# Optimization experiments

Measured on AMD Instinct MI355X. Metric: run time of the kernel, lower is better.

Reference implementation:

```python
import jax, jax.numpy as jnp
import numpy as np

IN_SIZE = 256
OUT_SIZE = 256
WIN = 2  # window_size


def setup_inputs() -> dict:
    key = jax.random.key(0)
    k1, k2 = jax.random.split(key)
    x = jax.random.normal(k1, (8, 4096, IN_SIZE), dtype=jnp.float32)
    W = jax.random.normal(k2, (3 * OUT_SIZE, WIN * IN_SIZE), dtype=jnp.float32) * 0.05
    b = jnp.zeros((3 * OUT_SIZE,), dtype=jnp.float32)
    return {"x": x, "W": W, "b": b}


def reference(x, W, b):
    bsz, seq_len, _ = x.shape
    toks = [x]
    for i in range(WIN - 1):
        shifted = jnp.concatenate(
            [jnp.zeros((bsz, i + 1, IN_SIZE), x.dtype), x[:, : -(i + 1), :]], axis=1
        )
        toks.insert(0, shifted)
    xw = jnp.stack(toks, axis=2).reshape(bsz, seq_len, WIN * IN_SIZE)

    # Gated projection: z (update), f (forget), o (output)
    y = xw @ W.T + b  # (B, S, 3*OUT)
    z, f, o = jnp.split(y, 3, axis=2)
    z = jnp.tanh(z)
    f = jax.nn.sigmoid(f)

    # fo-pooling recurrence: c_t = f_t * c_{t-1} + (1 - f_t) * z_t
    def step(c, fz):
        ft, zt = fz
        c = ft * c + (1.0 - ft) * zt
        return c, c

    fz = (jnp.swapaxes(f, 0, 1), jnp.swapaxes(z, 0, 1))  # (S, B, OUT)
    c0 = jnp.zeros((bsz, OUT_SIZE), z.dtype)
    _, cs = jax.lax.scan(step, c0, fz)
    c = jnp.swapaxes(cs, 0, 1)  # (B, S, OUT)

    return jax.nn.sigmoid(o) * c
```

## Files before the change

### kernel.cpp

```cpp
#include <hip/hip_runtime.h>
#include <cstdint>
#include <cstddef>

#define BATCH  8
#define SEQ    4096
#define CHN    256
#define NQ     768
#define KTOT   512
#define TS     128
#define NCHUNK (SEQ/TS)
#define SROW   4097

typedef __attribute__((ext_vector_type(8))) __bf16    bf16x8;
typedef __attribute__((ext_vector_type(4))) float     f32x4;
typedef __attribute__((ext_vector_type(4))) _Float16  f16x4;
typedef __attribute__((ext_vector_type(2))) _Float16  f16x2;

#define AS1(p) ((const __attribute__((address_space(1))) void*)(p))
#define AS3(p) ((__attribute__((address_space(3))) void*)(p))

__global__ __launch_bounds__(256) void k_convW(const float* __restrict__ W,
                                               __bf16* __restrict__ Wt) {
    int lin = blockIdx.x * 256 + threadIdx.x;
    int n  = lin % NQ;
    int tg = lin / NQ;
    const float* src = W + (size_t)n * KTOT + tg * 8;
    float4 a = *(const float4*)(src);
    float4 b = *(const float4*)(src + 4);
    bf16x8 h;
    h[0]=(__bf16)a.x; h[1]=(__bf16)a.y; h[2]=(__bf16)a.z; h[3]=(__bf16)a.w;
    h[4]=(__bf16)b.x; h[5]=(__bf16)b.y; h[6]=(__bf16)b.z; h[7]=(__bf16)b.w;
    *(bf16x8*)(Wt + (size_t)lin * 8) = h;
}

__global__ __launch_bounds__(256) void k_convX(const float* __restrict__ x,
                                               __bf16* __restrict__ Xb) {
    int c = blockIdx.x * 256 + threadIdx.x;
    if (c < 8 * 32) {
        int bz = c >> 5, j = c & 31;
        bf16x8 zz = {};
        *(bf16x8*)(Xb + (size_t)bz * SROW * 256 + j * 8) = zz;
    }
    int bi = c >> 17;
    int r  = c & 131071;
    int s  = r >> 5;
    int j  = r & 31;
    const float* src = x + ((size_t)bi * SEQ + s) * 256 + j * 8;
    float4 a = *(const float4*)(src);
    float4 b = *(const float4*)(src + 4);
    bf16x8 h;
    h[0]=(__bf16)a.x; h[1]=(__bf16)a.y; h[2]=(__bf16)a.z; h[3]=(__bf16)a.w;
    h[4]=(__bf16)b.x; h[5]=(__bf16)b.y; h[6]=(__bf16)b.z; h[7]=(__bf16)b.w;
    *(bf16x8*)(Xb + ((size_t)bi * SROW + 1 + s) * 256 + j * 8) = h;
}

__device__ __forceinline__ float fast_sigmoid(float y) {
    float e = __expf(-y);
    return __builtin_amdgcn_rcpf(1.f + e);
}
__device__ __forceinline__ float fast_tanh(float y) {
    float e = __expf(-2.f * y);
    return __builtin_amdgcn_rcpf(1.f + e) * 2.f - 1.f;
}

__global__ __launch_bounds__(256, 3) void k_gemm(
    const __bf16* __restrict__ Xb, const __bf16* __restrict__ Wt,
    const float* __restrict__ bias,
    _Float16* __restrict__ Zb, _Float16* __restrict__ Fb, _Float16* __restrict__ Ob)
{
    __shared__ char XL[2][16384];
    __shared__ char WL[2][8192];

    int tid = threadIdx.x;
    int bid = blockIdx.x;
    int x_  = bid & 7;
    int i_  = bid >> 3;
    int ngt = i_ % 6;
    int sbt = (i_ / 6) * 8 + x_;
    int bi  = sbt >> 5;
    int sc  = sbt & 31;
    int s0  = sc * 128;
    int wid = tid >> 6;
    int l   = tid & 63;
    int l15 = l & 15, lg = l >> 4;
    int wr  = wid >> 1;
    int wc  = wid & 1;

    #define STAGE_X(bsel, q)                                                     \
        {                                                                        \
            _Pragma("unroll")                                                    \
            for (int i2 = 0; i2 < 4; ++i2) {                                     \
                int slot = i2 * 256 + tid;                                       \
                int row  = slot >> 3;                                            \
                int c16  = slot & 7;                                             \
                int c16g = c16 ^ (row & 7);                                      \
                const __bf16* gsrc = Xb +                                        \
                    ((size_t)bi * SROW + s0 + row + ((q) >> 2)) * 256            \
                    + ((q) & 3) * 64 + c16g * 8;                                 \
                __builtin_amdgcn_global_load_lds(AS1(gsrc),                      \
                    AS3(XL[bsel] + slot * 16), 16, 0, 0);                        \
            }                                                                    \
        }
    #define STAGE_W(bsel, t)                                                     \
        {                                                                        \
            _Pragma("unroll")                                                    \
            for (int i2 = 0; i2 < 2; ++i2) {                                     \
                int slot = i2 * 256 + tid;                                       \
                int p  = slot >> 7;                                              \
                int nl = slot & 127;                                             \
                const __bf16* gsrc = Wt +                                        \
                    ((size_t)((t) * 4 + p) * NQ + ngt * 128 + nl) * 8;           \
                __builtin_amdgcn_global_load_lds(AS1(gsrc),                      \
                    AS3(WL[bsel] + slot * 16), 16, 0, 0);                        \
            }                                                                    \
        }

    f32x4 acc[4][4];
    const f32x4 vzero = {0.f, 0.f, 0.f, 0.f};
    #pragma unroll
    for (int a = 0; a < 4; ++a)
        #pragma unroll
        for (int b = 0; b < 4; ++b)
            acc[a][b] = vzero;

    STAGE_X(0, 0);
    STAGE_W(0, 0);
    __syncthreads();

    #pragma unroll
    for (int t = 0; t < 16; ++t) {
        if (t < 15) {
            STAGE_W((t + 1) & 1, t + 1);
            if (t & 1) STAGE_X(((t + 1) >> 1) & 1, (t + 1) >> 1);
        }

        const char* Xc = XL[(t >> 1) & 1];
        const char* Wc = WL[t & 1];
        bf16x8 xf[4], wf[4];
        #pragma unroll
        for (int st = 0; st < 4; ++st) {
            int row = wr * 64 + st * 16 + l15;
            int byte = (row * 128 + ((t & 1) * 4 + lg) * 16) ^ ((row & 7) << 4);
            xf[st] = *(const bf16x8*)(Xc + byte);
        }
        #pragma unroll
        for (int nt = 0; nt < 4; ++nt)
            wf[nt] = *(const bf16x8*)(Wc + lg * 2048
                                         + (wc * 64 + nt * 16 + l15) * 16);
        __builtin_amdgcn_s_setprio(1);
        #pragma unroll
        for (int nt = 0; nt < 4; ++nt)
            #pragma unroll
            for (int st = 0; st < 4; ++st)
                acc[nt][st] = __builtin_amdgcn_mfma_f32_16x16x32_bf16(
                                  wf[nt], xf[st], acc[nt][st], 0, 0, 0);
        __builtin_amdgcn_s_setprio(0);

        __syncthreads();
    }

    int gate    = ngt >> 1;
    int ch_base = (ngt & 1) * 128 + wc * 64;
    _Float16* buf = (gate == 0) ? Zb : (gate == 1) ? Fb : Ob;
    char* Sw = (char*)XL + wid * 8192;

    #pragma unroll
    for (int nt = 0; nt < 4; ++nt) {
        float4 bv = *(const float4*)(bias + ngt * 128 + wc * 64 + nt * 16 + lg * 4);
        #pragma unroll
        for (int st = 0; st < 4; ++st) {
            f16x4 hv;
            #pragma unroll
            for (int r = 0; r < 4; ++r) {
                float bvr = (r == 0) ? bv.x : (r == 1) ? bv.y : (r == 2) ? bv.z : bv.w;
                float y = acc[nt][st][r] + bvr;
                float v = (gate == 0) ? fast_tanh(y) : fast_sigmoid(y);
                hv[r] = (_Float16)v;
            }
            int byte = ((st * 16 + l15) * 128 + (nt * 16 + lg * 4) * 2)
                       ^ ((l15 & 7) << 4);
            *(f16x4*)(Sw + byte) = hv;
        }
    }
    #pragma unroll
    for (int so = 0; so < 16; ++so) {
        int s_loc = so * 4 + lg;
        int byte  = (s_loc * 128 + l15 * 8) ^ ((s_loc & 7) << 4);
        f16x4 v = *(const f16x4*)(Sw + byte);
        *(f16x4*)(buf + ((size_t)bi * SEQ + s0 + wr * 64 + s_loc) * CHN
                      + ch_base + l15 * 4) = v;
    }
}

__global__ __launch_bounds__(128) void k_scan1(const _Float16* __restrict__ Fb,
                                               const _Float16* __restrict__ Zb,
                                               float* __restrict__ Aq,
                                               float* __restrict__ Bq) {
    int bi = blockIdx.x >> 5;
    int ck = blockIdx.x & 31;
    int c2 = threadIdx.x;
    size_t base = (((size_t)bi * SEQ + ck * TS) * CHN + c2 * 2) >> 1;
    const f16x2* F2 = (const f16x2*)Fb;
    const f16x2* Z2 = (const f16x2*)Zb;
    float a0 = 1.f, a1 = 1.f, c0 = 0.f, c1 = 0.f;
    #pragma unroll 8
    for (int s = 0; s < TS; ++s) {
        f16x2 f = F2[base + (size_t)s * (CHN / 2)];
        f16x2 z = Z2[base + (size_t)s * (CHN / 2)];
        float f0 = (float)f[0], f1 = (float)f[1];
        c0 = f0 * c0 + (1.f - f0) * (float)z[0];
        c1 = f1 * c1 + (1.f - f1) * (float)z[1];
        a0 *= f0; a1 *= f1;
    }
    int o = blockIdx.x * CHN + c2 * 2;
    *(float2*)(Aq + o) = make_float2(a0, a1);
    *(float2*)(Bq + o) = make_float2(c0, c1);
}

__global__ __launch_bounds__(256) void k_scan2(const float* __restrict__ Aq,
                                               const float* __restrict__ Bq,
                                               float* __restrict__ Cq) {
    int bi = blockIdx.x;
    int ch = threadIdx.x;
    float c = 0.f;
    #pragma unroll
    for (int ck = 0; ck < NCHUNK; ++ck) {
        int o = (bi * NCHUNK + ck) * CHN + ch;
        Cq[o] = c;
        c = Aq[o] * c + Bq[o];
    }
}

__global__ __launch_bounds__(128) void k_scan3(const _Float16* __restrict__ Fb,
                                               const _Float16* __restrict__ Zb,
                                               const _Float16* __restrict__ Ob,
                                               const float* __restrict__ Cq,
                                               float* __restrict__ out) {
    int bi = blockIdx.x >> 5;
    int ck = blockIdx.x & 31;
    int c2 = threadIdx.x;
    float2 c = *(const float2*)(Cq + blockIdx.x * CHN + c2 * 2);
    size_t base = (((size_t)bi * SEQ + ck * TS) * CHN + c2 * 2) >> 1;
    const f16x2* F2 = (const f16x2*)Fb;
    const f16x2* Z2 = (const f16x2*)Zb;
    const f16x2* O2 = (const f16x2*)Ob;
    float* outp = out + (((size_t)bi * SEQ + ck * TS) * CHN + c2 * 2);
    #pragma unroll 4
    for (int s = 0; s < TS; ++s) {
        f16x2 f  = F2[base + (size_t)s * (CHN / 2)];
        f16x2 z  = Z2[base + (size_t)s * (CHN / 2)];
        f16x2 so = O2[base + (size_t)s * (CHN / 2)];
        float f0 = (float)f[0], f1 = (float)f[1];
        c.x = f0 * c.x + (1.f - f0) * (float)z[0];
        c.y = f1 * c.y + (1.f - f1) * (float)z[1];
        *(float2*)(outp + (size_t)s * CHN) = make_float2((float)so[0] * c.x,
                                                         (float)so[1] * c.y);
    }
}

extern "C" void kernel_launch(void* const* d_in, const int* in_sizes, int n_in,
                              void* d_out, int out_size, void* d_ws, size_t ws_size,
                              hipStream_t stream)
{
    const float* x = (const float*)d_in[0];
    const float* W = (const float*)d_in[1];
    const float* b = (const float*)d_in[2];
    float* out = (float*)d_out;

    char* ws = (char*)d_ws;
    const size_t MB = 1024 * 1024;
    _Float16* Zb = (_Float16*)(ws +  0 * MB);
    _Float16* Fb = (_Float16*)(ws + 16 * MB);
    _Float16* Ob = (_Float16*)(ws + 32 * MB);
    __bf16*   Wt = (__bf16*)  (ws + 48 * MB);
    float*    Aq = (float*)   (ws + 49 * MB);
    float*    Bq = (float*)   (ws + 50 * MB);
    float*    Cq = (float*)   (ws + 51 * MB);
    __bf16*   Xb = (__bf16*)  (ws + 52 * MB);

    k_convW<<<dim3(192),            dim3(256), 0, stream>>>(W, Wt);
    k_convX<<<dim3(4096),           dim3(256), 0, stream>>>(x, Xb);
    k_gemm <<<dim3(1536),           dim3(256), 0, stream>>>(Xb, Wt, b, Zb, Fb, Ob);
    k_scan1<<<dim3(BATCH * NCHUNK), dim3(128), 0, stream>>>(Fb, Zb, Aq, Bq);
    k_scan2<<<dim3(BATCH),          dim3(256), 0, stream>>>(Aq, Bq, Cq);
    k_scan3<<<dim3(BATCH * NCHUNK), dim3(128), 0, stream>>>(Fb, Zb, Ob, Cq, out);
}
```

Baseline: 78.72 us.

## Fuse fp32-to-bf16 X conversion into GEMM staging and halve sequence tile

Removes the separate X conversion kernel. The GEMM now loads fp32 x directly into registers, handles the shifted window with a zero row at the sequence start, converts to bf16 and writes the result to LDS after the MFMAs. The sequence tile is halved to 64 rows, which doubles the GEMM grid and the scan chunk count, and launch bounds are raised to 4 blocks per CU. This saves an intermediate bf16 buffer round trip and a launch. In exchange the X path goes through registers instead of direct global-to-LDS loads, global traffic per tile is doubled, and each block has a smaller MFMA tile with more W reloads.

```diff
diff --git a/kernel.cpp b/kernel.cpp
--- a/kernel.cpp
+++ b/kernel.cpp
@@ -7,9 +7,8 @@
 #define CHN    256
 #define NQ     768
 #define KTOT   512
-#define TS     128
+#define TS     64
 #define NCHUNK (SEQ/TS)
-#define SROW   4097
 
 typedef __attribute__((ext_vector_type(8))) __bf16    bf16x8;
 typedef __attribute__((ext_vector_type(4))) float     f32x4;
@@ -33,27 +32,6 @@
     *(bf16x8*)(Wt + (size_t)lin * 8) = h;
 }
 
-__global__ __launch_bounds__(256) void k_convX(const float* __restrict__ x,
-                                               __bf16* __restrict__ Xb) {
-    int c = blockIdx.x * 256 + threadIdx.x;
-    if (c < 8 * 32) {
-        int bz = c >> 5, j = c & 31;
-        bf16x8 zz = {};
-        *(bf16x8*)(Xb + (size_t)bz * SROW * 256 + j * 8) = zz;
-    }
-    int bi = c >> 17;
-    int r  = c & 131071;
-    int s  = r >> 5;
-    int j  = r & 31;
-    const float* src = x + ((size_t)bi * SEQ + s) * 256 + j * 8;
-    float4 a = *(const float4*)(src);
-    float4 b = *(const float4*)(src + 4);
-    bf16x8 h;
-    h[0]=(__bf16)a.x; h[1]=(__bf16)a.y; h[2]=(__bf16)a.z; h[3]=(__bf16)a.w;
-    h[4]=(__bf16)b.x; h[5]=(__bf16)b.y; h[6]=(__bf16)b.z; h[7]=(__bf16)b.w;
-    *(bf16x8*)(Xb + ((size_t)bi * SROW + 1 + s) * 256 + j * 8) = h;
-}
-
 __device__ __forceinline__ float fast_sigmoid(float y) {
     float e = __expf(-y);
     return __builtin_amdgcn_rcpf(1.f + e);
@@ -63,12 +41,12 @@
     return __builtin_amdgcn_rcpf(1.f + e) * 2.f - 1.f;
 }
 
-__global__ __launch_bounds__(256, 3) void k_gemm(
-    const __bf16* __restrict__ Xb, const __bf16* __restrict__ Wt,
+__global__ __launch_bounds__(256, 4) void k_gemm(
+    const float* __restrict__ x, const __bf16* __restrict__ Wt,
     const float* __restrict__ bias,
     _Float16* __restrict__ Zb, _Float16* __restrict__ Fb, _Float16* __restrict__ Ob)
 {
-    __shared__ char XL[2][16384];
+    __shared__ char XL[2][8192];
     __shared__ char WL[2][8192];
 
     int tid = threadIdx.x;
@@ -77,53 +55,65 @@
     int i_  = bid >> 3;
     int ngt = i_ % 6;
     int sbt = (i_ / 6) * 8 + x_;
-    int bi  = sbt >> 5;
-    int sc  = sbt & 31;
-    int s0  = sc * 128;
+    int bi  = sbt >> 6;
+    int sc  = sbt & 63;
+    int s0  = sc * 64;
     int wid = tid >> 6;
     int l   = tid & 63;
     int l15 = l & 15, lg = l >> 4;
     int wr  = wid >> 1;
     int wc  = wid & 1;
 
-    #define STAGE_X(bsel, q)                                                     \
-        {                                                                        \
-            _Pragma("unroll")                                                    \
-            for (int i2 = 0; i2 < 4; ++i2) {                                     \
-                int slot = i2 * 256 + tid;                                       \
-                int row  = slot >> 3;                                            \
-                int c16  = slot & 7;                                             \
-                int c16g = c16 ^ (row & 7);                                      \
-                const __bf16* gsrc = Xb +                                        \
-                    ((size_t)bi * SROW + s0 + row + ((q) >> 2)) * 256            \
-                    + ((q) & 3) * 64 + c16g * 8;                                 \
-                __builtin_amdgcn_global_load_lds(AS1(gsrc),                      \
-                    AS3(XL[bsel] + slot * 16), 16, 0, 0);                        \
-            }                                                                    \
-        }
+    float4 xa[2], xb[2];
+    #define XLOAD(q)                                                             \
+        { _Pragma("unroll")                                                      \
+          for (int i2 = 0; i2 < 2; ++i2) {                                       \
+              int slot = i2 * 256 + tid;                                         \
+              int row  = slot >> 3;                                              \
+              int c16g = (slot & 7) ^ (row & 7);                                 \
+              int row_x = s0 + row + ((q) >> 2) - 1;                             \
+              if (row_x >= 0) {                                                  \
+                  const float* src = x + ((size_t)bi * SEQ + row_x) * 256        \
+                                       + ((q) & 3) * 64 + c16g * 8;              \
+                  xa[i2] = *(const float4*)src;                                  \
+                  xb[i2] = *(const float4*)(src + 4);                            \
+              } else {                                                           \
+                  xa[i2] = make_float4(0.f, 0.f, 0.f, 0.f);                      \
+                  xb[i2] = xa[i2];                                               \
+              }                                                                  \
+          } }
+    #define XWRITE(bsel)                                                         \
+        { _Pragma("unroll")                                                      \
+          for (int i2 = 0; i2 < 2; ++i2) {                                       \
+              int slot = i2 * 256 + tid;                                         \
+              bf16x8 h;                                                          \
+              h[0]=(__bf16)xa[i2].x; h[1]=(__bf16)xa[i2].y;                      \
+              h[2]=(__bf16)xa[i2].z; h[3]=(__bf16)xa[i2].w;                      \
+              h[4]=(__bf16)xb[i2].x; h[5]=(__bf16)xb[i2].y;                      \
+              h[6]=(__bf16)xb[i2].z; h[7]=(__bf16)xb[i2].w;                      \
+              *(bf16x8*)(XL[bsel] + slot * 16) = h;                              \
+          } }
     #define STAGE_W(bsel, t)                                                     \
-        {                                                                        \
-            _Pragma("unroll")                                                    \
-            for (int i2 = 0; i2 < 2; ++i2) {                                     \
-                int slot = i2 * 256 + tid;                                       \
-                int p  = slot >> 7;                                              \
-                int nl = slot & 127;                                             \
-                const __bf16* gsrc = Wt +                                        \
-                    ((size_t)((t) * 4 + p) * NQ + ngt * 128 + nl) * 8;           \
-                __builtin_amdgcn_global_load_lds(AS1(gsrc),                      \
-                    AS3(WL[bsel] + slot * 16), 16, 0, 0);                        \
-            }                                                                    \
-        }
-
-    f32x4 acc[4][4];
+        { _Pragma("unroll")                                                      \
+          for (int i2 = 0; i2 < 2; ++i2) {                                       \
+              int slot = i2 * 256 + tid;                                         \
+              int p  = slot >> 7;                                                \
+              int nl = slot & 127;                                               \
+              const __bf16* gsrc = Wt +                                          \
+                  ((size_t)((t) * 4 + p) * NQ + ngt * 128 + nl) * 8;             \
+              __builtin_amdgcn_global_load_lds(AS1(gsrc),                        \
+                  AS3(WL[bsel] + slot * 16), 16, 0, 0);                          \
+          } }
+
+    f32x4 acc[4][2];
     const f32x4 vzero = {0.f, 0.f, 0.f, 0.f};
     #pragma unroll
     for (int a = 0; a < 4; ++a)
         #pragma unroll
-        for (int b = 0; b < 4; ++b)
+        for (int b = 0; b < 2; ++b)
             acc[a][b] = vzero;
 
-    STAGE_X(0, 0);
+    XLOAD(0); XWRITE(0);
     STAGE_W(0, 0);
     __syncthreads();
 
@@ -131,15 +121,15 @@
     for (int t = 0; t < 16; ++t) {
         if (t < 15) {
             STAGE_W((t + 1) & 1, t + 1);
-            if (t & 1) STAGE_X(((t + 1) >> 1) & 1, (t + 1) >> 1);
+            if (t & 1) XLOAD((t + 1) >> 1);
         }
 
         const char* Xc = XL[(t >> 1) & 1];
         const char* Wc = WL[t & 1];
-        bf16x8 xf[4], wf[4];
-        #pragma unroll
-        for (int st = 0; st < 4; ++st) {
-            int row = wr * 64 + st * 16 + l15;
+        bf16x8 xf[2], wf[4];
+        #pragma unroll
+        for (int st = 0; st < 2; ++st) {
+            int row = wr * 32 + st * 16 + l15;
             int byte = (row * 128 + ((t & 1) * 4 + lg) * 16) ^ ((row & 7) << 4);
             xf[st] = *(const bf16x8*)(Xc + byte);
         }
@@ -147,28 +137,30 @@
         for (int nt = 0; nt < 4; ++nt)
             wf[nt] = *(const bf16x8*)(Wc + lg * 2048
                                          + (wc * 64 + nt * 16 + l15) * 16);
-        __builtin_amdgcn_s_setprio(1);
         #pragma unroll
         for (int nt = 0; nt < 4; ++nt)
             #pragma unroll
-            for (int st = 0; st < 4; ++st)
+            for (int st = 0; st < 2; ++st)
                 acc[nt][st] = __builtin_amdgcn_mfma_f32_16x16x32_bf16(
                                   wf[nt], xf[st], acc[nt][st], 0, 0, 0);
-        __builtin_amdgcn_s_setprio(0);
+
+        if ((t & 1) && t < 15) XWRITE(((t + 1) >> 1) & 1);
 
         __syncthreads();
     }
+
+    __syncthreads();
 
     int gate    = ngt >> 1;
     int ch_base = (ngt & 1) * 128 + wc * 64;
     _Float16* buf = (gate == 0) ? Zb : (gate == 1) ? Fb : Ob;
-    char* Sw = (char*)XL + wid * 8192;
+    char* Sw = (char*)XL + wid * 4096;
 
     #pragma unroll
     for (int nt = 0; nt < 4; ++nt) {
         float4 bv = *(const float4*)(bias + ngt * 128 + wc * 64 + nt * 16 + lg * 4);
         #pragma unroll
-        for (int st = 0; st < 4; ++st) {
+        for (int st = 0; st < 2; ++st) {
             f16x4 hv;
             #pragma unroll
             for (int r = 0; r < 4; ++r) {
@@ -183,11 +175,11 @@
         }
     }
     #pragma unroll
-    for (int so = 0; so < 16; ++so) {
+    for (int so = 0; so < 8; ++so) {
         int s_loc = so * 4 + lg;
         int byte  = (s_loc * 128 + l15 * 8) ^ ((s_loc & 7) << 4);
         f16x4 v = *(const f16x4*)(Sw + byte);
-        *(f16x4*)(buf + ((size_t)bi * SEQ + s0 + wr * 64 + s_loc) * CHN
+        *(f16x4*)(buf + ((size_t)bi * SEQ + s0 + wr * 32 + s_loc) * CHN
                       + ch_base + l15 * 4) = v;
     }
 }
@@ -196,8 +188,8 @@
                                                const _Float16* __restrict__ Zb,
                                                float* __restrict__ Aq,
                                                float* __restrict__ Bq) {
-    int bi = blockIdx.x >> 5;
-    int ck = blockIdx.x & 31;
+    int bi = blockIdx.x >> 6;
+    int ck = blockIdx.x & 63;
     int c2 = threadIdx.x;
     size_t base = (((size_t)bi * SEQ + ck * TS) * CHN + c2 * 2) >> 1;
     const f16x2* F2 = (const f16x2*)Fb;
@@ -236,8 +228,8 @@
                                                const _Float16* __restrict__ Ob,
                                                const float* __restrict__ Cq,
                                                float* __restrict__ out) {
-    int bi = blockIdx.x >> 5;
-    int ck = blockIdx.x & 31;
+    int bi = blockIdx.x >> 6;
+    int ck = blockIdx.x & 63;
     int c2 = threadIdx.x;
     float2 c = *(const float2*)(Cq + blockIdx.x * CHN + c2 * 2);
     size_t base = (((size_t)bi * SEQ + ck * TS) * CHN + c2 * 2) >> 1;
@@ -276,11 +268,9 @@
     float*    Aq = (float*)   (ws + 49 * MB);
     float*    Bq = (float*)   (ws + 50 * MB);
     float*    Cq = (float*)   (ws + 51 * MB);
-    __bf16*   Xb = (__bf16*)  (ws + 52 * MB);
 
     k_convW<<<dim3(192),            dim3(256), 0, stream>>>(W, Wt);
-    k_convX<<<dim3(4096),           dim3(256), 0, stream>>>(x, Xb);
-    k_gemm <<<dim3(1536),           dim3(256), 0, stream>>>(Xb, Wt, b, Zb, Fb, Ob);
+    k_gemm <<<dim3(3072),           dim3(256), 0, stream>>>(x, Wt, b, Zb, Fb, Ob);
     k_scan1<<<dim3(BATCH * NCHUNK), dim3(128), 0, stream>>>(Fb, Zb, Aq, Bq);
     k_scan2<<<dim3(BATCH),          dim3(256), 0, stream>>>(Aq, Bq, Cq);
     k_scan3<<<dim3(BATCH * NCHUNK), dim3(128), 0, stream>>>(Fb, Zb, Ob, Cq, out);
```

Result: slower. 81.45 us (+3.5%).
